# Kernel optimization log

Hardware: AMD Instinct MI355X
Metric: run time of the kernel (lower is better)

## Reference

```python
import jax, jax.numpy as jnp
from jax import lax
import numpy as np

T, B, DIN, NQ = 256, 2048, 128, 16  # hidden_dim == n_qubits (required by module math)


def setup_inputs() -> dict:
    key = jax.random.key(0)
    k1, k2, k3 = jax.random.split(key, 3)
    inputs = jax.random.normal(k1, (T, B, DIN), dtype=jnp.float32)
    # stacked params for the 4 gates: forget, input, update, output
    W = jax.random.normal(k2, (4, NQ, DIN + NQ), dtype=jnp.float32) * 0.1
    b = jnp.zeros((4, NQ), dtype=jnp.float32)
    theta = jax.random.normal(k3, (4, NQ), dtype=jnp.float32)
    return {"inputs": inputs, "W": W, "b": b, "theta": theta}


def reference(inputs, W, b, theta):
    # Analytic simulation of each QGate circuit:
    #   RX(x_i) then RX(theta_i) on wire i  ->  product state, <Z_i> = cos(x_i + theta_i)
    #   CNOT chain (0->1, 1->2, ...): Heisenberg picture maps Z_k -> Z_0 Z_1 ... Z_k,
    Tn, Bn, _ = inputs.shape
    nq = theta.shape[-1]
    h0 = jnp.zeros((Bn, nq), dtype=inputs.dtype)
    c0 = jnp.zeros((Bn, nq), dtype=inputs.dtype)

    def step(carry, x):
        hx, cx = carry
        combined = jnp.concatenate([x, hx], axis=1)              # [B, Din+H]
        z = jnp.einsum('bd,gnd->bgn', combined, W) + b           # [B, 4, nq]
        q = jnp.cumprod(jnp.cos(z + theta), axis=-1)             # quantum gate expectations
        f = jax.nn.sigmoid(q[:, 0])
        i = jax.nn.sigmoid(q[:, 1])
        g = jnp.tanh(q[:, 2])
        o = jax.nn.sigmoid(q[:, 3])
        cx = f * cx + i * g
        hx = o * jnp.tanh(cx)
        return (hx, cx), hx

    (hx, cx), outputs = lax.scan(step, (h0, c0), inputs)
    return outputs, hx, cx
```

## Files before the change

### kernel.cpp

```cpp
#include <hip/hip_runtime.h>
#include <hip/hip_bf16.h>
#include <stdint.h>


#define T_STEPS 256
#define BATCH   2048
#define DIN     128
#define NQ      16
#define DTOT    144
#define NTILE   16
#define ZROW    66

typedef __attribute__((ext_vector_type(8))) short bf16x8;
typedef __attribute__((ext_vector_type(4))) float f32x4;
typedef __attribute__((ext_vector_type(2))) int   int2v;

#if defined(__has_builtin)
#if __has_builtin(__builtin_amdgcn_permlane16_swap) && __has_builtin(__builtin_amdgcn_permlane32_swap)
#define USE_PLSWAP 1
#endif
#endif
#ifndef USE_PLSWAP
#define USE_PLSWAP 0
#endif

__device__ __forceinline__ float bf2f(unsigned short u) {
    union { unsigned int i; float f; } v; v.i = ((unsigned int)u) << 16; return v.f;
}
__device__ __forceinline__ unsigned short f2bf(float f) {
    union { float f; unsigned int i; } v; v.f = f;
    unsigned int i = v.i;
    unsigned int r = i + 0x7fffu + ((i >> 16) & 1u);
    return (unsigned short)(r >> 16);
}
__device__ __forceinline__ float ldval(const float* p) { return *p; }
__device__ __forceinline__ float ldval(const unsigned short* p) { return bf2f(*p); }

__device__ __forceinline__ int detect_bf16(const unsigned int* __restrict__ xw, int lane) {
    int cnt = 0;
#pragma unroll
    for (int i = 0; i < 4; ++i) {
        unsigned int w = xw[lane + i * 64];
        unsigned int e = (w >> 7) & 0xFFu;
        cnt += (e >= 100u && e <= 140u) ? 1 : 0;
    }
#pragma unroll
    for (int d = 32; d > 0; d >>= 1) cnt += __shfl_down(cnt, d, 64);
    int tot = __shfl(cnt, 0, 64);
    return (tot >= 140) ? 1 : 0;
}

template <int BASE>
__device__ __forceinline__ void qstep(int t, int g, int n, float cur,
                                      const float (&Wp)[16], float& h, float& c,
                                      float& hsave, float* __restrict__ out, int b,
                                      bool m0, bool m1,
                                      int a_f, int a_i, int a_g, int a_o)
{
    float a0 = cur, a1, a2, a3;
    asm volatile(
        "s_nop 1\n\t"
        "v_fmac_f32 %0, %4, %5\n\t"
        "v_mul_f32_dpp %1, %4, %6 row_ror:4 row_mask:0xf bank_mask:0xf\n\t"
        "v_mul_f32_dpp %2, %4, %7 row_ror:8 row_mask:0xf bank_mask:0xf\n\t"
        "v_mul_f32_dpp %3, %4, %8 row_ror:12 row_mask:0xf bank_mask:0xf\n\t"
        "v_fmac_f32_dpp %0, %4, %9 row_ror:1 row_mask:0xf bank_mask:0xf\n\t"
        "v_fmac_f32_dpp %1, %4, %10 row_ror:5 row_mask:0xf bank_mask:0xf\n\t"
        "v_fmac_f32_dpp %2, %4, %11 row_ror:9 row_mask:0xf bank_mask:0xf\n\t"
        "v_fmac_f32_dpp %3, %4, %12 row_ror:13 row_mask:0xf bank_mask:0xf\n\t"
        "v_fmac_f32_dpp %0, %4, %13 row_ror:2 row_mask:0xf bank_mask:0xf\n\t"
        "v_fmac_f32_dpp %1, %4, %14 row_ror:6 row_mask:0xf bank_mask:0xf\n\t"
        "v_fmac_f32_dpp %2, %4, %15 row_ror:10 row_mask:0xf bank_mask:0xf\n\t"
        "v_fmac_f32_dpp %3, %4, %16 row_ror:14 row_mask:0xf bank_mask:0xf\n\t"
        "v_fmac_f32_dpp %0, %4, %17 row_ror:3 row_mask:0xf bank_mask:0xf\n\t"
        "v_fmac_f32_dpp %1, %4, %18 row_ror:7 row_mask:0xf bank_mask:0xf\n\t"
        "v_fmac_f32_dpp %2, %4, %19 row_ror:11 row_mask:0xf bank_mask:0xf\n\t"
        "v_fmac_f32_dpp %3, %4, %20 row_ror:15 row_mask:0xf bank_mask:0xf"
        : "+v"(a0), "=&v"(a1), "=&v"(a2), "=&v"(a3)
        : "v"(h), "v"(Wp[0]), "v"(Wp[4]), "v"(Wp[8]), "v"(Wp[12]),
          "v"(Wp[1]), "v"(Wp[5]), "v"(Wp[9]), "v"(Wp[13]),
          "v"(Wp[2]), "v"(Wp[6]), "v"(Wp[10]), "v"(Wp[14]),
          "v"(Wp[3]), "v"(Wp[7]), "v"(Wp[11]), "v"(Wp[15]));
    float z = (a0 + a1) + (a2 + a3);

    float cz = __cosf(z);
    if constexpr (BASE == 0x110) {
        asm volatile(
            "s_nop 1\n\t"
            "v_mul_f32_dpp %0, %0, %0 row_shr:1 row_mask:0xf bank_mask:0xf\n\t"
            "s_nop 1\n\t"
            "v_mul_f32_dpp %0, %0, %0 row_shr:2 row_mask:0xf bank_mask:0xf\n\t"
            "s_nop 1\n\t"
            "v_mul_f32_dpp %0, %0, %0 row_shr:4 row_mask:0xf bank_mask:0xf\n\t"
            "s_nop 1\n\t"
            "v_mul_f32_dpp %0, %0, %0 row_shr:8 row_mask:0xf bank_mask:0xf"
            : "+v"(cz));
    } else {
        asm volatile(
            "s_nop 1\n\t"
            "v_mul_f32_dpp %0, %0, %0 row_shl:1 row_mask:0xf bank_mask:0xf\n\t"
            "s_nop 1\n\t"
            "v_mul_f32_dpp %0, %0, %0 row_shl:2 row_mask:0xf bank_mask:0xf\n\t"
            "s_nop 1\n\t"
            "v_mul_f32_dpp %0, %0, %0 row_shl:4 row_mask:0xf bank_mask:0xf\n\t"
            "s_nop 1\n\t"
            "v_mul_f32_dpp %0, %0, %0 row_shl:8 row_mask:0xf bank_mask:0xf"
            : "+v"(cz));
    }

    float a = (g == 2) ? 2.f * cz : cz;
    float e = __expf(-a);
    float rr = __builtin_amdgcn_rcpf(1.f + e);
    float s = (g == 2) ? (1.f - e) * rr : rr;

    float fv, iv, gv, ov;
#if USE_PLSWAP
    int si = __builtin_bit_cast(int, s);
    int2v e1 = __builtin_amdgcn_permlane16_swap(si, si, false, false);
    int c1i = m0 ? e1[0] : e1[1];
    int2v e2 = __builtin_amdgcn_permlane32_swap(si, si, false, false);
    int c2i = m1 ? e2[0] : e2[1];
    int2v e3 = __builtin_amdgcn_permlane16_swap(c2i, c2i, false, false);
    int c3i = m0 ? e3[0] : e3[1];
    float C0 = s;
    float C1 = __builtin_bit_cast(float, c1i);
    float C2 = __builtin_bit_cast(float, c2i);
    float C3 = __builtin_bit_cast(float, c3i);
    float P  = m1 ? C2 : C0;
    float Q  = m1 ? C3 : C1;
    float R_ = m1 ? C0 : C2;
    float S_ = m1 ? C1 : C3;
    fv = m0 ? Q  : P;
    iv = m0 ? P  : Q;
    gv = m0 ? S_ : R_;
    ov = m0 ? R_ : S_;
#else
    int si = __builtin_bit_cast(int, s);
    fv = __builtin_bit_cast(float, __builtin_amdgcn_ds_bpermute(a_f, si));
    iv = __builtin_bit_cast(float, __builtin_amdgcn_ds_bpermute(a_i, si));
    gv = __builtin_bit_cast(float, __builtin_amdgcn_ds_bpermute(a_g, si));
    ov = __builtin_bit_cast(float, __builtin_amdgcn_ds_bpermute(a_o, si));
#endif

    c = fmaf(fv, c, iv * gv);
    float e2t = __expf(-2.f * c);
    float tc = (1.f - e2t) * __builtin_amdgcn_rcpf(1.f + e2t);
    h = ov * tc;

    if ((t & 3) == g) hsave = h;
    if ((t & 3) == 3)
        out[(size_t)(t - 3 + g) * (BATCH * NQ) + (size_t)b * NQ + n] = hsave;
}

template <int BASE, typename InT>
__device__ __forceinline__ void fused_main(
    const InT* __restrict__ x, const InT* __restrict__ W,
    const InT* __restrict__ bv, const InT* __restrict__ th,
    float* __restrict__ out, int b, int w, int lane,
    const float (&Wp)[16], float (*zt)[ZROW],
    bf16x8 (*wfh)[64], bf16x8 (*wfl)[64])
{
    const int m = lane & 15, quad = lane >> 4;
    const int g = quad, n = m;
    const bool m0 = (g & 1) != 0, m1 = (g & 2) != 0;
    const int a_f = n << 2, a_i = (16 + n) << 2, a_g = (32 + n) << 2, a_o = (48 + n) << 2;

    if constexpr (sizeof(InT) == 2) {
#pragma unroll
        for (int nb = 0; nb < 4; ++nb)
            wfh[w * 4 + nb][lane] = *(const bf16x8*)((const unsigned short*)W +
                                    (size_t)(nb * 16 + m) * DTOT + w * 32 + quad * 8);
    } else {
#pragma unroll
        for (int nb = 0; nb < 4; ++nb) {
            const float* p = (const float*)W + (size_t)(nb * 16 + m) * DTOT + w * 32 + quad * 8;
            bf16x8 ah, al;
#pragma unroll
            for (int j = 0; j < 8; ++j) {
                float wv = p[j];
                unsigned short hh = f2bf(wv);
                ah[j] = (short)hh;
                al[j] = (short)f2bf(wv - bf2f(hh));
            }
            wfh[w * 4 + nb][lane] = ah;
            wfl[w * 4 + nb][lane] = al;
        }
    }
    const float bias = ldval(bv + lane) + ldval(th + lane);
    __syncthreads();

    const InT* xbase = x + ((size_t)m * BATCH + (size_t)b) * DIN + quad * 8;

    f32x4 rx[8]; bf16x8 rbx[4];
    auto LOAD = [&](int tl) {
        const InT* p = xbase + (size_t)tl * ((size_t)16 * BATCH * DIN);
#pragma unroll
        for (int kt = 0; kt < 4; ++kt) {
            if constexpr (sizeof(InT) == 2) {
                rbx[kt] = *(const bf16x8*)(p + kt * 32);
            } else {
                rx[2 * kt]     = *(const f32x4*)((const float*)p + kt * 32);
                rx[2 * kt + 1] = *(const f32x4*)((const float*)p + kt * 32 + 4);
            }
        }
    };
    auto PRODUCE = [&]() {
        f32x4 acc[4] = {};
#pragma unroll
        for (int kt = 0; kt < 4; ++kt) {
            if constexpr (sizeof(InT) == 2) {
#pragma unroll
                for (int nb = 0; nb < 4; ++nb)
                    acc[nb] = __builtin_amdgcn_mfma_f32_16x16x32_bf16(rbx[kt], wfh[kt * 4 + nb][lane], acc[nb], 0, 0, 0);
            } else {
                bf16x8 ah, al;
#pragma unroll
                for (int j = 0; j < 8; ++j) {
                    float xv = rx[2 * kt + (j >> 2)][j & 3];
                    unsigned short hh = f2bf(xv);
                    ah[j] = (short)hh;
                    al[j] = (short)f2bf(xv - bf2f(hh));
                }
#pragma unroll
                for (int nb = 0; nb < 4; ++nb)
                    acc[nb] = __builtin_amdgcn_mfma_f32_16x16x32_bf16(ah, wfh[kt * 4 + nb][lane], acc[nb], 0, 0, 0);
#pragma unroll
                for (int nb = 0; nb < 4; ++nb)
                    acc[nb] = __builtin_amdgcn_mfma_f32_16x16x32_bf16(al, wfh[kt * 4 + nb][lane], acc[nb], 0, 0, 0);
#pragma unroll
                for (int nb = 0; nb < 4; ++nb)
                    acc[nb] = __builtin_amdgcn_mfma_f32_16x16x32_bf16(ah, wfl[kt * 4 + nb][lane], acc[nb], 0, 0, 0);
            }
        }
#pragma unroll
        for (int nb = 0; nb < 4; ++nb)
#pragma unroll
            for (int r = 0; r < 4; ++r)
                zt[quad * 4 + r][nb * 16 + m] = acc[nb][r];
    };

    float h = 0.f, c = 0.f, hsave = 0.f;

    LOAD(0);
    PRODUCE();
    LOAD(1);

#pragma unroll 1
    for (int tl = 0; tl < NTILE; ++tl) {
        const int t0 = tl * 16;
        float zr[16];
#pragma unroll
        for (int j = 0; j < 16; ++j) zr[j] = zt[j][lane] + bias;
        if (tl < NTILE - 1) PRODUCE();
        if (tl < NTILE - 2) LOAD(tl + 2);
#pragma unroll
        for (int j = 0; j < 16; ++j)
            qstep<BASE>(t0 + j, g, n, zr[j], Wp, h, c, hsave, out, b, m0, m1, a_f, a_i, a_g, a_o);
    }

    if (g == 0) {
        out[(size_t)T_STEPS * BATCH * NQ + (size_t)b * NQ + n] = h;
        out[(size_t)T_STEPS * BATCH * NQ + (size_t)BATCH * NQ + (size_t)b * NQ + n] = c;
    }
}

__global__ __launch_bounds__(256, 2) void qlstm_fused(
    const void* __restrict__ x_, const void* __restrict__ W_,
    const void* __restrict__ b_, const void* __restrict__ th_,
    float* __restrict__ out)
{
    __shared__ float  zw[4][NTILE][ZROW];
    __shared__ bf16x8 wfh[16][64];
    __shared__ bf16x8 wfl[16][64];

    const int lane = threadIdx.x & 63;
    const int w    = threadIdx.x >> 6;
    const int b    = blockIdx.x * 4 + w;
    const int n    = lane & 15;

    const int isbf = __builtin_amdgcn_readfirstlane(detect_bf16((const unsigned int*)x_, lane));

    int pr  = __builtin_amdgcn_update_dpp(0, lane, 0x121, 0xF, 0xF, false);
    int p0r = __shfl(pr, 0, 64);
    const int d = (p0r == 1) ? 1 : 15;

    float Wp[16];
    if (isbf) {
        const unsigned short* W = (const unsigned short*)W_;
#pragma unroll
        for (int k = 0; k < 16; ++k)
            Wp[k] = bf2f(W[(size_t)lane * DTOT + DIN + ((n + k * d) & 15)]);
    } else {
        const float* W = (const float*)W_;
#pragma unroll
        for (int k = 0; k < 16; ++k)
            Wp[k] = W[(size_t)lane * DTOT + DIN + ((n + k * d) & 15)];
    }

    int probe = __builtin_amdgcn_update_dpp(999, lane, 0x111, 0xF, 0xF, false);
    int p2 = __shfl(probe, 2, 64);

    if (isbf) {
        if (p2 == 1) fused_main<0x110, unsigned short>((const unsigned short*)x_, (const unsigned short*)W_,
                                                       (const unsigned short*)b_, (const unsigned short*)th_,
                                                       out, b, w, lane, Wp, zw[w], wfh, wfl);
        else         fused_main<0x100, unsigned short>((const unsigned short*)x_, (const unsigned short*)W_,
                                                       (const unsigned short*)b_, (const unsigned short*)th_,
                                                       out, b, w, lane, Wp, zw[w], wfh, wfl);
    } else {
        if (p2 == 1) fused_main<0x110, float>((const float*)x_, (const float*)W_,
                                              (const float*)b_, (const float*)th_,
                                              out, b, w, lane, Wp, zw[w], wfh, wfl);
        else         fused_main<0x100, float>((const float*)x_, (const float*)W_,
                                              (const float*)b_, (const float*)th_,
                                              out, b, w, lane, Wp, zw[w], wfh, wfl);
    }
}

extern "C" void kernel_launch(void* const* d_in, const int* in_sizes, int n_in,
                              void* d_out, int out_size, void* d_ws, size_t ws_size,
                              hipStream_t stream) {
    const void* x  = d_in[0];
    const void* W  = d_in[1];
    const void* bv = d_in[2];
    const void* th = d_in[3];
    (void)d_ws; (void)ws_size;
    qlstm_fused<<<BATCH / 4, 256, 0, stream>>>(x, W, bv, th, (float*)d_out);
}
```

Before: 388.7 us.

## Process two batch rows per wavefront with interleaved recurrent chains

Each wavefront now carries two independent batch elements (A and B) through the recurrence. Their DPP matvec, cumprod, activation and gate-exchange instructions are interleaved so one chain's work fills the other's dependency stalls, and the s_nops between dependent DPP ops are dropped. The input tile is re-laid out to 8 timesteps × 2 batch rows per 16-row tile, the grid is halved, and launch bounds drop to one block per SIMD-pair hint. Sigmoid/tanh are also rewritten with exp2 and a per-lane scale/offset to remove selects. This trades lower occupancy and more registers for higher instruction-level parallelism in the latency-bound serial loop.

```diff
diff --git a/kernel.cpp b/kernel.cpp
--- a/kernel.cpp
+++ b/kernel.cpp
@@ -8,7 +8,7 @@
 #define DIN     128
 #define NQ      16
 #define DTOT    144
-#define NTILE   16
+#define NTILE   32
 #define ZROW    66
 
 typedef __attribute__((ext_vector_type(8))) short bf16x8;
@@ -50,70 +50,10 @@
     return (tot >= 140) ? 1 : 0;
 }
 
-template <int BASE>
-__device__ __forceinline__ void qstep(int t, int g, int n, float cur,
-                                      const float (&Wp)[16], float& h, float& c,
-                                      float& hsave, float* __restrict__ out, int b,
-                                      bool m0, bool m1,
-                                      int a_f, int a_i, int a_g, int a_o)
+__device__ __forceinline__ void gex(float s, bool m0, bool m1,
+                                    int a_f, int a_i, int a_g, int a_o,
+                                    float& fv, float& iv, float& gv, float& ov)
 {
-    float a0 = cur, a1, a2, a3;
-    asm volatile(
-        "s_nop 1\n\t"
-        "v_fmac_f32 %0, %4, %5\n\t"
-        "v_mul_f32_dpp %1, %4, %6 row_ror:4 row_mask:0xf bank_mask:0xf\n\t"
-        "v_mul_f32_dpp %2, %4, %7 row_ror:8 row_mask:0xf bank_mask:0xf\n\t"
-        "v_mul_f32_dpp %3, %4, %8 row_ror:12 row_mask:0xf bank_mask:0xf\n\t"
-        "v_fmac_f32_dpp %0, %4, %9 row_ror:1 row_mask:0xf bank_mask:0xf\n\t"
-        "v_fmac_f32_dpp %1, %4, %10 row_ror:5 row_mask:0xf bank_mask:0xf\n\t"
-        "v_fmac_f32_dpp %2, %4, %11 row_ror:9 row_mask:0xf bank_mask:0xf\n\t"
-        "v_fmac_f32_dpp %3, %4, %12 row_ror:13 row_mask:0xf bank_mask:0xf\n\t"
-        "v_fmac_f32_dpp %0, %4, %13 row_ror:2 row_mask:0xf bank_mask:0xf\n\t"
-        "v_fmac_f32_dpp %1, %4, %14 row_ror:6 row_mask:0xf bank_mask:0xf\n\t"
-        "v_fmac_f32_dpp %2, %4, %15 row_ror:10 row_mask:0xf bank_mask:0xf\n\t"
-        "v_fmac_f32_dpp %3, %4, %16 row_ror:14 row_mask:0xf bank_mask:0xf\n\t"
-        "v_fmac_f32_dpp %0, %4, %17 row_ror:3 row_mask:0xf bank_mask:0xf\n\t"
-        "v_fmac_f32_dpp %1, %4, %18 row_ror:7 row_mask:0xf bank_mask:0xf\n\t"
-        "v_fmac_f32_dpp %2, %4, %19 row_ror:11 row_mask:0xf bank_mask:0xf\n\t"
-        "v_fmac_f32_dpp %3, %4, %20 row_ror:15 row_mask:0xf bank_mask:0xf"
-        : "+v"(a0), "=&v"(a1), "=&v"(a2), "=&v"(a3)
-        : "v"(h), "v"(Wp[0]), "v"(Wp[4]), "v"(Wp[8]), "v"(Wp[12]),
-          "v"(Wp[1]), "v"(Wp[5]), "v"(Wp[9]), "v"(Wp[13]),
-          "v"(Wp[2]), "v"(Wp[6]), "v"(Wp[10]), "v"(Wp[14]),
-          "v"(Wp[3]), "v"(Wp[7]), "v"(Wp[11]), "v"(Wp[15]));
-    float z = (a0 + a1) + (a2 + a3);
-
-    float cz = __cosf(z);
-    if constexpr (BASE == 0x110) {
-        asm volatile(
-            "s_nop 1\n\t"
-            "v_mul_f32_dpp %0, %0, %0 row_shr:1 row_mask:0xf bank_mask:0xf\n\t"
-            "s_nop 1\n\t"
-            "v_mul_f32_dpp %0, %0, %0 row_shr:2 row_mask:0xf bank_mask:0xf\n\t"
-            "s_nop 1\n\t"
-            "v_mul_f32_dpp %0, %0, %0 row_shr:4 row_mask:0xf bank_mask:0xf\n\t"
-            "s_nop 1\n\t"
-            "v_mul_f32_dpp %0, %0, %0 row_shr:8 row_mask:0xf bank_mask:0xf"
-            : "+v"(cz));
-    } else {
-        asm volatile(
-            "s_nop 1\n\t"
-            "v_mul_f32_dpp %0, %0, %0 row_shl:1 row_mask:0xf bank_mask:0xf\n\t"
-            "s_nop 1\n\t"
-            "v_mul_f32_dpp %0, %0, %0 row_shl:2 row_mask:0xf bank_mask:0xf\n\t"
-            "s_nop 1\n\t"
-            "v_mul_f32_dpp %0, %0, %0 row_shl:4 row_mask:0xf bank_mask:0xf\n\t"
-            "s_nop 1\n\t"
-            "v_mul_f32_dpp %0, %0, %0 row_shl:8 row_mask:0xf bank_mask:0xf"
-            : "+v"(cz));
-    }
-
-    float a = (g == 2) ? 2.f * cz : cz;
-    float e = __expf(-a);
-    float rr = __builtin_amdgcn_rcpf(1.f + e);
-    float s = (g == 2) ? (1.f - e) * rr : rr;
-
-    float fv, iv, gv, ov;
 #if USE_PLSWAP
     int si = __builtin_bit_cast(int, s);
     int2v e1 = __builtin_amdgcn_permlane16_swap(si, si, false, false);
@@ -141,28 +81,134 @@
     gv = __builtin_bit_cast(float, __builtin_amdgcn_ds_bpermute(a_g, si));
     ov = __builtin_bit_cast(float, __builtin_amdgcn_ds_bpermute(a_o, si));
 #endif
-
-    c = fmaf(fv, c, iv * gv);
-    float e2t = __expf(-2.f * c);
-    float tc = (1.f - e2t) * __builtin_amdgcn_rcpf(1.f + e2t);
-    h = ov * tc;
-
-    if ((t & 3) == g) hsave = h;
-    if ((t & 3) == 3)
-        out[(size_t)(t - 3 + g) * (BATCH * NQ) + (size_t)b * NQ + n] = hsave;
+}
+
+template <int BASE>
+__device__ __forceinline__ void qstep2(int t, int g, int n,
+                                       float curA, float curB, const float (&Wp)[16],
+                                       float& hA, float& cA, float& hsA, int bA,
+                                       float& hB, float& cB, float& hsB, int bB,
+                                       bool m0, bool m1,
+                                       float kexp, float ksc, float koff,
+                                       int a_f, int a_i, int a_g, int a_o,
+                                       float* __restrict__ out)
+{
+    float a0A = curA, a1A, a2A, a3A;
+    float a0B = curB, a1B, a2B, a3B;
+    asm volatile(
+        "s_nop 1\n\t"
+        "v_fmac_f32 %0, %8, %10\n\t"
+        "v_fmac_f32 %4, %9, %10\n\t"
+        "v_mul_f32_dpp %1, %8, %11 row_ror:4 row_mask:0xf bank_mask:0xf\n\t"
+        "v_mul_f32_dpp %5, %9, %11 row_ror:4 row_mask:0xf bank_mask:0xf\n\t"
+        "v_mul_f32_dpp %2, %8, %12 row_ror:8 row_mask:0xf bank_mask:0xf\n\t"
+        "v_mul_f32_dpp %6, %9, %12 row_ror:8 row_mask:0xf bank_mask:0xf\n\t"
+        "v_mul_f32_dpp %3, %8, %13 row_ror:12 row_mask:0xf bank_mask:0xf\n\t"
+        "v_mul_f32_dpp %7, %9, %13 row_ror:12 row_mask:0xf bank_mask:0xf\n\t"
+        "v_fmac_f32_dpp %0, %8, %14 row_ror:1 row_mask:0xf bank_mask:0xf\n\t"
+        "v_fmac_f32_dpp %4, %9, %14 row_ror:1 row_mask:0xf bank_mask:0xf\n\t"
+        "v_fmac_f32_dpp %1, %8, %15 row_ror:5 row_mask:0xf bank_mask:0xf\n\t"
+        "v_fmac_f32_dpp %5, %9, %15 row_ror:5 row_mask:0xf bank_mask:0xf\n\t"
+        "v_fmac_f32_dpp %2, %8, %16 row_ror:9 row_mask:0xf bank_mask:0xf\n\t"
+        "v_fmac_f32_dpp %6, %9, %16 row_ror:9 row_mask:0xf bank_mask:0xf\n\t"
+        "v_fmac_f32_dpp %3, %8, %17 row_ror:13 row_mask:0xf bank_mask:0xf\n\t"
+        "v_fmac_f32_dpp %7, %9, %17 row_ror:13 row_mask:0xf bank_mask:0xf\n\t"
+        "v_fmac_f32_dpp %0, %8, %18 row_ror:2 row_mask:0xf bank_mask:0xf\n\t"
+        "v_fmac_f32_dpp %4, %9, %18 row_ror:2 row_mask:0xf bank_mask:0xf\n\t"
+        "v_fmac_f32_dpp %1, %8, %19 row_ror:6 row_mask:0xf bank_mask:0xf\n\t"
+        "v_fmac_f32_dpp %5, %9, %19 row_ror:6 row_mask:0xf bank_mask:0xf\n\t"
+        "v_fmac_f32_dpp %2, %8, %20 row_ror:10 row_mask:0xf bank_mask:0xf\n\t"
+        "v_fmac_f32_dpp %6, %9, %20 row_ror:10 row_mask:0xf bank_mask:0xf\n\t"
+        "v_fmac_f32_dpp %3, %8, %21 row_ror:14 row_mask:0xf bank_mask:0xf\n\t"
+        "v_fmac_f32_dpp %7, %9, %21 row_ror:14 row_mask:0xf bank_mask:0xf\n\t"
+        "v_fmac_f32_dpp %0, %8, %22 row_ror:3 row_mask:0xf bank_mask:0xf\n\t"
+        "v_fmac_f32_dpp %4, %9, %22 row_ror:3 row_mask:0xf bank_mask:0xf\n\t"
+        "v_fmac_f32_dpp %1, %8, %23 row_ror:7 row_mask:0xf bank_mask:0xf\n\t"
+        "v_fmac_f32_dpp %5, %9, %23 row_ror:7 row_mask:0xf bank_mask:0xf\n\t"
+        "v_fmac_f32_dpp %2, %8, %24 row_ror:11 row_mask:0xf bank_mask:0xf\n\t"
+        "v_fmac_f32_dpp %6, %9, %24 row_ror:11 row_mask:0xf bank_mask:0xf\n\t"
+        "v_fmac_f32_dpp %3, %8, %25 row_ror:15 row_mask:0xf bank_mask:0xf\n\t"
+        "v_fmac_f32_dpp %7, %9, %25 row_ror:15 row_mask:0xf bank_mask:0xf"
+        : "+v"(a0A), "=&v"(a1A), "=&v"(a2A), "=&v"(a3A),
+          "+v"(a0B), "=&v"(a1B), "=&v"(a2B), "=&v"(a3B)
+        : "v"(hA), "v"(hB),
+          "v"(Wp[0]), "v"(Wp[4]), "v"(Wp[8]), "v"(Wp[12]),
+          "v"(Wp[1]), "v"(Wp[5]), "v"(Wp[9]), "v"(Wp[13]),
+          "v"(Wp[2]), "v"(Wp[6]), "v"(Wp[10]), "v"(Wp[14]),
+          "v"(Wp[3]), "v"(Wp[7]), "v"(Wp[11]), "v"(Wp[15]));
+    float zA = (a0A + a1A) + (a2A + a3A);
+    float zB = (a0B + a1B) + (a2B + a3B);
+
+    float czA = __cosf(zA);
+    float czB = __cosf(zB);
+    if constexpr (BASE == 0x110) {
+        asm volatile(
+            "s_nop 1\n\t"
+            "v_mul_f32_dpp %0, %0, %0 row_shr:1 row_mask:0xf bank_mask:0xf\n\t"
+            "v_mul_f32_dpp %1, %1, %1 row_shr:1 row_mask:0xf bank_mask:0xf\n\t"
+            "v_mul_f32_dpp %0, %0, %0 row_shr:2 row_mask:0xf bank_mask:0xf\n\t"
+            "v_mul_f32_dpp %1, %1, %1 row_shr:2 row_mask:0xf bank_mask:0xf\n\t"
+            "v_mul_f32_dpp %0, %0, %0 row_shr:4 row_mask:0xf bank_mask:0xf\n\t"
+            "v_mul_f32_dpp %1, %1, %1 row_shr:4 row_mask:0xf bank_mask:0xf\n\t"
+            "v_mul_f32_dpp %0, %0, %0 row_shr:8 row_mask:0xf bank_mask:0xf\n\t"
+            "v_mul_f32_dpp %1, %1, %1 row_shr:8 row_mask:0xf bank_mask:0xf"
+            : "+v"(czA), "+v"(czB));
+    } else {
+        asm volatile(
+            "s_nop 1\n\t"
+            "v_mul_f32_dpp %0, %0, %0 row_shl:1 row_mask:0xf bank_mask:0xf\n\t"
+            "v_mul_f32_dpp %1, %1, %1 row_shl:1 row_mask:0xf bank_mask:0xf\n\t"
+            "v_mul_f32_dpp %0, %0, %0 row_shl:2 row_mask:0xf bank_mask:0xf\n\t"
+            "v_mul_f32_dpp %1, %1, %1 row_shl:2 row_mask:0xf bank_mask:0xf\n\t"
+            "v_mul_f32_dpp %0, %0, %0 row_shl:4 row_mask:0xf bank_mask:0xf\n\t"
+            "v_mul_f32_dpp %1, %1, %1 row_shl:4 row_mask:0xf bank_mask:0xf\n\t"
+            "v_mul_f32_dpp %0, %0, %0 row_shl:8 row_mask:0xf bank_mask:0xf\n\t"
+            "v_mul_f32_dpp %1, %1, %1 row_shl:8 row_mask:0xf bank_mask:0xf"
+            : "+v"(czA), "+v"(czB));
+    }
+
+    float eA = __builtin_amdgcn_exp2f(czA * kexp);
+    float eB = __builtin_amdgcn_exp2f(czB * kexp);
+    float rrA = __builtin_amdgcn_rcpf(1.f + eA);
+    float rrB = __builtin_amdgcn_rcpf(1.f + eB);
+    float sA = fmaf(ksc, rrA, koff);
+    float sB = fmaf(ksc, rrB, koff);
+
+    float fvA, ivA, gvA, ovA, fvB, ivB, gvB, ovB;
+    gex(sA, m0, m1, a_f, a_i, a_g, a_o, fvA, ivA, gvA, ovA);
+    gex(sB, m0, m1, a_f, a_i, a_g, a_o, fvB, ivB, gvB, ovB);
+
+    cA = fmaf(fvA, cA, ivA * gvA);
+    cB = fmaf(fvB, cB, ivB * gvB);
+    float e2A = __builtin_amdgcn_exp2f(cA * -2.885390082f);
+    float e2B = __builtin_amdgcn_exp2f(cB * -2.885390082f);
+    float tcA = fmaf(2.f, __builtin_amdgcn_rcpf(1.f + e2A), -1.f);
+    float tcB = fmaf(2.f, __builtin_amdgcn_rcpf(1.f + e2B), -1.f);
+    hA = ovA * tcA;
+    hB = ovB * tcB;
+
+    if ((t & 3) == g) { hsA = hA; hsB = hB; }
+    if ((t & 3) == 3) {
+        out[(size_t)(t - 3 + g) * (BATCH * NQ) + (size_t)bA * NQ + n] = hsA;
+        out[(size_t)(t - 3 + g) * (BATCH * NQ) + (size_t)bB * NQ + n] = hsB;
+    }
 }
 
 template <int BASE, typename InT>
 __device__ __forceinline__ void fused_main(
     const InT* __restrict__ x, const InT* __restrict__ W,
     const InT* __restrict__ bv, const InT* __restrict__ th,
-    float* __restrict__ out, int b, int w, int lane,
+    float* __restrict__ out, int bA, int w, int lane,
     const float (&Wp)[16], float (*zt)[ZROW],
     bf16x8 (*wfh)[64], bf16x8 (*wfl)[64])
 {
     const int m = lane & 15, quad = lane >> 4;
     const int g = quad, n = m;
+    const int bB = bA + 1;
     const bool m0 = (g & 1) != 0, m1 = (g & 2) != 0;
+    const float kexp = (g == 2) ? -2.885390082f : -1.442695041f;
+    const float ksc  = (g == 2) ? 2.f : 1.f;
+    const float koff = (g == 2) ? -1.f : 0.f;
     const int a_f = n << 2, a_i = (16 + n) << 2, a_g = (32 + n) << 2, a_o = (48 + n) << 2;
 
     if constexpr (sizeof(InT) == 2) {
@@ -189,11 +235,11 @@
     const float bias = ldval(bv + lane) + ldval(th + lane);
     __syncthreads();
 
-    const InT* xbase = x + ((size_t)m * BATCH + (size_t)b) * DIN + quad * 8;
+    const InT* xbase = x + ((size_t)(m & 7) * BATCH + (size_t)(bA + (m >> 3))) * DIN + quad * 8;
 
     f32x4 rx[8]; bf16x8 rbx[4];
     auto LOAD = [&](int tl) {
-        const InT* p = xbase + (size_t)tl * ((size_t)16 * BATCH * DIN);
+        const InT* p = xbase + (size_t)tl * ((size_t)8 * BATCH * DIN);
 #pragma unroll
         for (int kt = 0; kt < 4; ++kt) {
             if constexpr (sizeof(InT) == 2) {
@@ -239,7 +285,8 @@
                 zt[quad * 4 + r][nb * 16 + m] = acc[nb][r];
     };
 
-    float h = 0.f, c = 0.f, hsave = 0.f;
+    float hA = 0.f, cA = 0.f, hsA = 0.f;
+    float hB = 0.f, cB = 0.f, hsB = 0.f;
 
     LOAD(0);
     PRODUCE();
@@ -247,35 +294,41 @@
 
 #pragma unroll 1
     for (int tl = 0; tl < NTILE; ++tl) {
-        const int t0 = tl * 16;
-        float zr[16];
-#pragma unroll
-        for (int j = 0; j < 16; ++j) zr[j] = zt[j][lane] + bias;
+        const int t0 = tl * 8;
+        float zrA[8], zrB[8];
+#pragma unroll
+        for (int j = 0; j < 8; ++j) zrA[j] = zt[j][lane] + bias;
+#pragma unroll
+        for (int j = 0; j < 8; ++j) zrB[j] = zt[8 + j][lane] + bias;
         if (tl < NTILE - 1) PRODUCE();
         if (tl < NTILE - 2) LOAD(tl + 2);
 #pragma unroll
-        for (int j = 0; j < 16; ++j)
-            qstep<BASE>(t0 + j, g, n, zr[j], Wp, h, c, hsave, out, b, m0, m1, a_f, a_i, a_g, a_o);
+        for (int j = 0; j < 8; ++j)
+            qstep2<BASE>(t0 + j, g, n, zrA[j], zrB[j], Wp,
+                         hA, cA, hsA, bA, hB, cB, hsB, bB,
+                         m0, m1, kexp, ksc, koff, a_f, a_i, a_g, a_o, out);
     }
 
     if (g == 0) {
-        out[(size_t)T_STEPS * BATCH * NQ + (size_t)b * NQ + n] = h;
-        out[(size_t)T_STEPS * BATCH * NQ + (size_t)BATCH * NQ + (size_t)b * NQ + n] = c;
-    }
-}
-
-__global__ __launch_bounds__(256, 2) void qlstm_fused(
+        out[(size_t)T_STEPS * BATCH * NQ + (size_t)bA * NQ + n] = hA;
+        out[(size_t)T_STEPS * BATCH * NQ + (size_t)BATCH * NQ + (size_t)bA * NQ + n] = cA;
+        out[(size_t)T_STEPS * BATCH * NQ + (size_t)bB * NQ + n] = hB;
+        out[(size_t)T_STEPS * BATCH * NQ + (size_t)BATCH * NQ + (size_t)bB * NQ + n] = cB;
+    }
+}
+
+__global__ __launch_bounds__(256, 1) void qlstm_fused(
     const void* __restrict__ x_, const void* __restrict__ W_,
     const void* __restrict__ b_, const void* __restrict__ th_,
     float* __restrict__ out)
 {
-    __shared__ float  zw[4][NTILE][ZROW];
+    __shared__ float  zw[4][16][ZROW];
     __shared__ bf16x8 wfh[16][64];
     __shared__ bf16x8 wfl[16][64];
 
     const int lane = threadIdx.x & 63;
     const int w    = threadIdx.x >> 6;
-    const int b    = blockIdx.x * 4 + w;
+    const int bA   = (blockIdx.x * 4 + w) * 2;
     const int n    = lane & 15;
 
     const int isbf = __builtin_amdgcn_readfirstlane(detect_bf16((const unsigned int*)x_, lane));
@@ -303,17 +356,17 @@
     if (isbf) {
         if (p2 == 1) fused_main<0x110, unsigned short>((const unsigned short*)x_, (const unsigned short*)W_,
                                                        (const unsigned short*)b_, (const unsigned short*)th_,
-                                                       out, b, w, lane, Wp, zw[w], wfh, wfl);
+                                                       out, bA, w, lane, Wp, zw[w], wfh, wfl);
         else         fused_main<0x100, unsigned short>((const unsigned short*)x_, (const unsigned short*)W_,
                                                        (const unsigned short*)b_, (const unsigned short*)th_,
-                                                       out, b, w, lane, Wp, zw[w], wfh, wfl);
+                                                       out, bA, w, lane, Wp, zw[w], wfh, wfl);
     } else {
         if (p2 == 1) fused_main<0x110, float>((const float*)x_, (const float*)W_,
                                               (const float*)b_, (const float*)th_,
-                                              out, b, w, lane, Wp, zw[w], wfh, wfl);
+                                              out, bA, w, lane, Wp, zw[w], wfh, wfl);
         else         fused_main<0x100, float>((const float*)x_, (const float*)W_,
                                               (const float*)b_, (const float*)th_,
-                                              out, b, w, lane, Wp, zw[w], wfh, wfl);
+                                              out, bA, w, lane, Wp, zw[w], wfh, wfl);
     }
 }
 
@@ -325,5 +378,5 @@
     const void* bv = d_in[2];
     const void* th = d_in[3];
     (void)d_ws; (void)ws_size;
-    qlstm_fused<<<BATCH / 4, 256, 0, stream>>>(x, W, bv, th, (float*)d_out);
-}
+    qlstm_fused<<<BATCH / 8, 256, 0, stream>>>(x, W, bv, th, (float*)d_out);
+}
```

After: 385.1 us. No clear change (-0.9%).

## Interleave two independent batch recurrences per wave to hide serial latency

Applied to the files above, without the earlier changes.

Each wave now runs the recurrence for two batch rows at once and staggers them, so one row's matvec and cos prefix product overlap the other row's gate activation and cell update. The goal is to fill the dependency stalls in the serial per-step chain. The time tile now holds 8 steps for each of two rows, the grid is halved, and launch bounds drop to one block per SM. Sigmoid and tanh are rewritten with exp2 and fma constants, and the DPP prefix product uses update_dpp builtins in place of inline asm. The cost is fewer waves in flight and more register pressure.

```diff
diff --git a/kernel.cpp b/kernel.cpp
--- a/kernel.cpp
+++ b/kernel.cpp
@@ -8,7 +8,7 @@
 #define DIN     128
 #define NQ      16
 #define DTOT    144
-#define NTILE   16
+#define NTILE   32
 #define ZROW    66
 
 typedef __attribute__((ext_vector_type(8))) short bf16x8;
@@ -50,13 +50,15 @@
     return (tot >= 140) ? 1 : 0;
 }
 
-template <int BASE>
-__device__ __forceinline__ void qstep(int t, int g, int n, float cur,
-                                      const float (&Wp)[16], float& h, float& c,
-                                      float& hsave, float* __restrict__ out, int b,
-                                      bool m0, bool m1,
-                                      int a_f, int a_i, int a_g, int a_o)
-{
+template <int CTRL>
+__device__ __forceinline__ float dpp_sh(float v) {
+    int r = __builtin_amdgcn_update_dpp(__builtin_bit_cast(int, 1.0f),
+                                        __builtin_bit_cast(int, v),
+                                        CTRL, 0xF, 0xF, false);
+    return __builtin_bit_cast(float, r);
+}
+
+__device__ __forceinline__ float dot1(float h, float cur, const float (&Wp)[16]) {
     float a0 = cur, a1, a2, a3;
     asm volatile(
         "s_nop 1\n\t"
@@ -81,39 +83,23 @@
           "v"(Wp[1]), "v"(Wp[5]), "v"(Wp[9]), "v"(Wp[13]),
           "v"(Wp[2]), "v"(Wp[6]), "v"(Wp[10]), "v"(Wp[14]),
           "v"(Wp[3]), "v"(Wp[7]), "v"(Wp[11]), "v"(Wp[15]));
-    float z = (a0 + a1) + (a2 + a3);
-
+    return (a0 + a1) + (a2 + a3);
+}
+
+template <int BASE>
+__device__ __forceinline__ float cosprefix(float z) {
     float cz = __cosf(z);
-    if constexpr (BASE == 0x110) {
-        asm volatile(
-            "s_nop 1\n\t"
-            "v_mul_f32_dpp %0, %0, %0 row_shr:1 row_mask:0xf bank_mask:0xf\n\t"
-            "s_nop 1\n\t"
-            "v_mul_f32_dpp %0, %0, %0 row_shr:2 row_mask:0xf bank_mask:0xf\n\t"
-            "s_nop 1\n\t"
-            "v_mul_f32_dpp %0, %0, %0 row_shr:4 row_mask:0xf bank_mask:0xf\n\t"
-            "s_nop 1\n\t"
-            "v_mul_f32_dpp %0, %0, %0 row_shr:8 row_mask:0xf bank_mask:0xf"
-            : "+v"(cz));
-    } else {
-        asm volatile(
-            "s_nop 1\n\t"
-            "v_mul_f32_dpp %0, %0, %0 row_shl:1 row_mask:0xf bank_mask:0xf\n\t"
-            "s_nop 1\n\t"
-            "v_mul_f32_dpp %0, %0, %0 row_shl:2 row_mask:0xf bank_mask:0xf\n\t"
-            "s_nop 1\n\t"
-            "v_mul_f32_dpp %0, %0, %0 row_shl:4 row_mask:0xf bank_mask:0xf\n\t"
-            "s_nop 1\n\t"
-            "v_mul_f32_dpp %0, %0, %0 row_shl:8 row_mask:0xf bank_mask:0xf"
-            : "+v"(cz));
-    }
-
-    float a = (g == 2) ? 2.f * cz : cz;
-    float e = __expf(-a);
-    float rr = __builtin_amdgcn_rcpf(1.f + e);
-    float s = (g == 2) ? (1.f - e) * rr : rr;
-
-    float fv, iv, gv, ov;
+    cz *= dpp_sh<BASE + 1>(cz);
+    cz *= dpp_sh<BASE + 2>(cz);
+    cz *= dpp_sh<BASE + 4>(cz);
+    cz *= dpp_sh<BASE + 8>(cz);
+    return cz;
+}
+
+__device__ __forceinline__ void gex(float s, bool m0, bool m1,
+                                    int a_f, int a_i, int a_g, int a_o,
+                                    float& fv, float& iv, float& gv, float& ov)
+{
 #if USE_PLSWAP
     int si = __builtin_bit_cast(int, s);
     int2v e1 = __builtin_amdgcn_permlane16_swap(si, si, false, false);
@@ -141,28 +127,47 @@
     gv = __builtin_bit_cast(float, __builtin_amdgcn_ds_bpermute(a_g, si));
     ov = __builtin_bit_cast(float, __builtin_amdgcn_ds_bpermute(a_o, si));
 #endif
+}
+
+__device__ __forceinline__ void tail1(int t, int g, int n, float cz,
+                                      float& h, float& c, float& hs, int b,
+                                      bool m0, bool m1,
+                                      float kexp, float ksc, float koff,
+                                      int a_f, int a_i, int a_g, int a_o,
+                                      float* __restrict__ out)
+{
+    float e = __builtin_amdgcn_exp2f(cz * kexp);
+    float rr = __builtin_amdgcn_rcpf(1.f + e);
+    float s = fmaf(ksc, rr, koff);
+
+    float fv, iv, gv, ov;
+    gex(s, m0, m1, a_f, a_i, a_g, a_o, fv, iv, gv, ov);
 
     c = fmaf(fv, c, iv * gv);
-    float e2t = __expf(-2.f * c);
-    float tc = (1.f - e2t) * __builtin_amdgcn_rcpf(1.f + e2t);
+    float e2 = __builtin_amdgcn_exp2f(c * -2.885390082f);
+    float tc = fmaf(2.f, __builtin_amdgcn_rcpf(1.f + e2), -1.f);
     h = ov * tc;
 
-    if ((t & 3) == g) hsave = h;
+    if ((t & 3) == g) hs = h;
     if ((t & 3) == 3)
-        out[(size_t)(t - 3 + g) * (BATCH * NQ) + (size_t)b * NQ + n] = hsave;
+        out[(size_t)(t - 3 + g) * (BATCH * NQ) + (size_t)b * NQ + n] = hs;
 }
 
 template <int BASE, typename InT>
 __device__ __forceinline__ void fused_main(
     const InT* __restrict__ x, const InT* __restrict__ W,
     const InT* __restrict__ bv, const InT* __restrict__ th,
-    float* __restrict__ out, int b, int w, int lane,
+    float* __restrict__ out, int bA, int w, int lane,
     const float (&Wp)[16], float (*zt)[ZROW],
     bf16x8 (*wfh)[64], bf16x8 (*wfl)[64])
 {
     const int m = lane & 15, quad = lane >> 4;
     const int g = quad, n = m;
+    const int bB = bA + 1;
     const bool m0 = (g & 1) != 0, m1 = (g & 2) != 0;
+    const float kexp = (g == 2) ? -2.885390082f : -1.442695041f;
+    const float ksc  = (g == 2) ? 2.f : 1.f;
+    const float koff = (g == 2) ? -1.f : 0.f;
     const int a_f = n << 2, a_i = (16 + n) << 2, a_g = (32 + n) << 2, a_o = (48 + n) << 2;
 
     if constexpr (sizeof(InT) == 2) {
@@ -189,11 +194,11 @@
     const float bias = ldval(bv + lane) + ldval(th + lane);
     __syncthreads();
 
-    const InT* xbase = x + ((size_t)m * BATCH + (size_t)b) * DIN + quad * 8;
+    const InT* xbase = x + ((size_t)(m & 7) * BATCH + (size_t)(bA + (m >> 3))) * DIN + quad * 8;
 
     f32x4 rx[8]; bf16x8 rbx[4];
     auto LOAD = [&](int tl) {
-        const InT* p = xbase + (size_t)tl * ((size_t)16 * BATCH * DIN);
+        const InT* p = xbase + (size_t)tl * ((size_t)8 * BATCH * DIN);
 #pragma unroll
         for (int kt = 0; kt < 4; ++kt) {
             if constexpr (sizeof(InT) == 2) {
@@ -239,43 +244,69 @@
                 zt[quad * 4 + r][nb * 16 + m] = acc[nb][r];
     };
 
-    float h = 0.f, c = 0.f, hsave = 0.f;
+    float hA = 0.f, cA = 0.f, hsA = 0.f;
+    float hB = 0.f, cB = 0.f, hsB = 0.f;
+    float zrA[8], zrB[8];
 
     LOAD(0);
     PRODUCE();
     LOAD(1);
+#pragma unroll
+    for (int j = 0; j < 8; ++j) zrA[j] = zt[j][lane] + bias;
+#pragma unroll
+    for (int j = 0; j < 8; ++j) zrB[j] = zt[8 + j][lane] + bias;
+
+    float zA = dot1(hA, zrA[0], Wp);
+    float czB = 0.f;
 
 #pragma unroll 1
     for (int tl = 0; tl < NTILE; ++tl) {
-        const int t0 = tl * 16;
-        float zr[16];
-#pragma unroll
-        for (int j = 0; j < 16; ++j) zr[j] = zt[j][lane] + bias;
         if (tl < NTILE - 1) PRODUCE();
         if (tl < NTILE - 2) LOAD(tl + 2);
 #pragma unroll
-        for (int j = 0; j < 16; ++j)
-            qstep<BASE>(t0 + j, g, n, zr[j], Wp, h, c, hsave, out, b, m0, m1, a_f, a_i, a_g, a_o);
-    }
+        for (int j = 0; j < 8; ++j) {
+            const int t = tl * 8 + j;
+            float czA = cosprefix<BASE>(zA);
+            if (j != 0 || tl != 0)
+                tail1(t - 1, g, n, czB, hB, cB, hsB, bB, m0, m1,
+                      kexp, ksc, koff, a_f, a_i, a_g, a_o, out);
+            float zB = dot1(hB, zrB[j], Wp);
+            czB = cosprefix<BASE>(zB);
+            tail1(t, g, n, czA, hA, cA, hsA, bA, m0, m1,
+                  kexp, ksc, koff, a_f, a_i, a_g, a_o, out);
+            if (j < 7) zA = dot1(hA, zrA[j + 1], Wp);
+        }
+        if (tl < NTILE - 1) {
+#pragma unroll
+            for (int j = 0; j < 8; ++j) zrA[j] = zt[j][lane] + bias;
+#pragma unroll
+            for (int j = 0; j < 8; ++j) zrB[j] = zt[8 + j][lane] + bias;
+            zA = dot1(hA, zrA[0], Wp);
+        }
+    }
+    tail1(T_STEPS - 1, g, n, czB, hB, cB, hsB, bB, m0, m1,
+          kexp, ksc, koff, a_f, a_i, a_g, a_o, out);
 
     if (g == 0) {
-        out[(size_t)T_STEPS * BATCH * NQ + (size_t)b * NQ + n] = h;
-        out[(size_t)T_STEPS * BATCH * NQ + (size_t)BATCH * NQ + (size_t)b * NQ + n] = c;
-    }
-}
-
-__global__ __launch_bounds__(256, 2) void qlstm_fused(
+        out[(size_t)T_STEPS * BATCH * NQ + (size_t)bA * NQ + n] = hA;
+        out[(size_t)T_STEPS * BATCH * NQ + (size_t)BATCH * NQ + (size_t)bA * NQ + n] = cA;
+        out[(size_t)T_STEPS * BATCH * NQ + (size_t)bB * NQ + n] = hB;
+        out[(size_t)T_STEPS * BATCH * NQ + (size_t)BATCH * NQ + (size_t)bB * NQ + n] = cB;
+    }
+}
+
+__global__ __launch_bounds__(256, 1) void qlstm_fused(
     const void* __restrict__ x_, const void* __restrict__ W_,
     const void* __restrict__ b_, const void* __restrict__ th_,
     float* __restrict__ out)
 {
-    __shared__ float  zw[4][NTILE][ZROW];
+    __shared__ float  zw[4][16][ZROW];
     __shared__ bf16x8 wfh[16][64];
     __shared__ bf16x8 wfl[16][64];
 
     const int lane = threadIdx.x & 63;
     const int w    = threadIdx.x >> 6;
-    const int b    = blockIdx.x * 4 + w;
+    const int bA   = (blockIdx.x * 4 + w) * 2;
     const int n    = lane & 15;
 
     const int isbf = __builtin_amdgcn_readfirstlane(detect_bf16((const unsigned int*)x_, lane));
@@ -303,17 +334,17 @@
     if (isbf) {
         if (p2 == 1) fused_main<0x110, unsigned short>((const unsigned short*)x_, (const unsigned short*)W_,
                                                        (const unsigned short*)b_, (const unsigned short*)th_,
-                                                       out, b, w, lane, Wp, zw[w], wfh, wfl);
+                                                       out, bA, w, lane, Wp, zw[w], wfh, wfl);
         else         fused_main<0x100, unsigned short>((const unsigned short*)x_, (const unsigned short*)W_,
                                                        (const unsigned short*)b_, (const unsigned short*)th_,
-                                                       out, b, w, lane, Wp, zw[w], wfh, wfl);
+                                                       out, bA, w, lane, Wp, zw[w], wfh, wfl);
     } else {
         if (p2 == 1) fused_main<0x110, float>((const float*)x_, (const float*)W_,
                                               (const float*)b_, (const float*)th_,
-                                              out, b, w, lane, Wp, zw[w], wfh, wfl);
+                                              out, bA, w, lane, Wp, zw[w], wfh, wfl);
         else         fused_main<0x100, float>((const float*)x_, (const float*)W_,
                                               (const float*)b_, (const float*)th_,
-                                              out, b, w, lane, Wp, zw[w], wfh, wfl);
+                                              out, bA, w, lane, Wp, zw[w], wfh, wfl);
     }
 }
 
@@ -325,5 +356,5 @@
     const void* bv = d_in[2];
     const void* th = d_in[3];
     (void)d_ws; (void)ws_size;
-    qlstm_fused<<<BATCH / 4, 256, 0, stream>>>(x, W, bv, th, (float*)d_out);
-}
+    qlstm_fused<<<BATCH / 8, 256, 0, stream>>>(x, W, bv, th, (float*)d_out);
+}
```

After: 390.9 us. About the same (+0.6%).
